# Kernel tuning notes

Measured on AMD Instinct MI355X. Metric: run time of the kernel, lower is better.

The kernel has to match this reference:

```python
import jax, jax.numpy as jnp
import numpy as np

DIM = 1024
N_HEADS = 16
HEAD_DIM = DIM // N_HEADS
SCALE = HEAD_DIM ** -0.5


def setup_inputs() -> dict:
    key = jax.random.key(0)
    ks = jax.random.split(key, 5)
    B, N = 2, 2048
    x = jax.random.normal(ks[0], (B, N, DIM), dtype=jnp.float32)
    # torch Linear: y = x @ W.T + b, W shape (out, in)
    qkv_w = jax.random.normal(ks[1], (3 * DIM, DIM), dtype=jnp.float32) * (DIM ** -0.5)
    qkv_b = jax.random.normal(ks[2], (3 * DIM,), dtype=jnp.float32) * 0.02
    proj_w = jax.random.normal(ks[3], (DIM, DIM), dtype=jnp.float32) * (DIM ** -0.5)
    proj_b = jax.random.normal(ks[4], (DIM,), dtype=jnp.float32) * 0.02
    return {"x": x, "qkv_w": qkv_w, "qkv_b": qkv_b, "proj_w": proj_w, "proj_b": proj_b}


def reference(x, qkv_w, qkv_b, proj_w, proj_b):
    B, N, D = x.shape
    qkv = x @ qkv_w.T + qkv_b                      # [B, N, 3D]
    qkv = qkv.reshape(B, N, 3, N_HEADS, HEAD_DIM)
    qkv = jnp.transpose(qkv, (2, 0, 3, 1, 4))      # [3, B, H, N, hd]
    q, k, v = qkv[0], qkv[1], qkv[2]
    dp = jnp.einsum('bhqd,bhkd->bhqk', q, k) * SCALE  # [B, H, N, N]
    attn = jax.nn.softmax(dp, axis=-1)
    wa = jnp.einsum('bhqk,bhkd->bhqd', attn, v)    # [B, H, N, hd]
    wa = jnp.transpose(wa, (0, 2, 1, 3)).reshape(B, N, D)
    return wa @ proj_w.T + proj_b
```

## Files before the change

kernel.cpp:

```cpp
#include <hip/hip_runtime.h>

#define BATCH 2
#define SEQ   2048
#define DIM   1024
#define NHEAD 16
#define HD    64
#define BH    (BATCH * NHEAD)
#define SCALE 0.125f
#define LOG2E 1.44269504f
#define NT    (SEQ / 64)

typedef __attribute__((ext_vector_type(8))) short short8;
typedef __attribute__((ext_vector_type(4))) float f32x4;

#define MFMA16(a, b, c) __builtin_amdgcn_mfma_f32_16x16x32_bf16(a, b, c, 0, 0, 0)

__device__ __forceinline__ ushort f2bf(float f) {
    union { float f; unsigned u; } v;
    v.f = f;
    unsigned r = (v.u + 0x7FFF + ((v.u >> 16) & 1)) >> 16;
    return (ushort)r;
}

__device__ __forceinline__ uint4 ld8f_bf16(const float* p) {
    float4 f0 = *(const float4*)p;
    float4 f1 = *(const float4*)(p + 4);
    union { ushort us[8]; uint4 v; } u;
    u.us[0] = f2bf(f0.x); u.us[1] = f2bf(f0.y);
    u.us[2] = f2bf(f0.z); u.us[3] = f2bf(f0.w);
    u.us[4] = f2bf(f1.x); u.us[5] = f2bf(f1.y);
    u.us[6] = f2bf(f1.z); u.us[7] = f2bf(f1.w);
    return u.v;
}

__device__ __forceinline__ void gl_lds16(const ushort* g, ushort* l) {
    __builtin_amdgcn_global_load_lds(
        (const __attribute__((address_space(1))) unsigned int*)g,
        (__attribute__((address_space(3))) unsigned int*)l,
        16, 0, 0);
}

#define N_X  (BATCH * SEQ * DIM)
#define N_QW (3 * DIM * DIM)
#define N_PW (DIM * DIM)

__global__ __launch_bounds__(256) void cvt_kernel(
    const float* __restrict__ x, const float* __restrict__ qw,
    const float* __restrict__ pw, ushort* __restrict__ xb,
    ushort* __restrict__ qwb, ushort* __restrict__ pwb)
{
    const int i = (blockIdx.x * 256 + threadIdx.x) * 8;
    if (i < N_X)  *(uint4*)(xb  + i) = ld8f_bf16(x  + i);
    if (i < N_QW) *(uint4*)(qwb + i) = ld8f_bf16(qw + i);
    if (i < N_PW) *(uint4*)(pwb + i) = ld8f_bf16(pw + i);
}

template <int MODE, int WM, typename TOUT>
__global__ __launch_bounds__(256, 2) void gemm_bt(
    const ushort* __restrict__ A, const ushort* __restrict__ W,
    const float* __restrict__ bias, TOUT* __restrict__ out,
    int M, int Nout, int K)
{
    constexpr int BM = 2 * WM * 16;
    __shared__ __align__(16) ushort As[2][BM * 32];
    __shared__ __align__(16) ushort Bs[2][128 * 32];

    const int tid  = threadIdx.x;
    const int wave = tid >> 6, lane = tid & 63;
    const int quad = lane >> 4, l16 = lane & 15;
    const int wm = wave >> 1, wn = wave & 1;
    const int m0 = blockIdx.y * BM, n0 = blockIdx.x * 128;

    const int c0 = tid, c1 = tid + 256;
    const ushort* gA0 = A + (size_t)(m0 + (c0 >> 2)) * K + (c0 & 3) * 8;
    const ushort* gA1 = A + (size_t)(m0 + (c1 >> 2)) * K + (c1 & 3) * 8;
    const ushort* gB0 = W + (size_t)(n0 + (c0 >> 2)) * K + (c0 & 3) * 8;
    const ushort* gB1 = W + (size_t)(n0 + (c1 >> 2)) * K + (c1 & 3) * 8;

#define STAGE_G(buf, k0)                                                  \
    {                                                                     \
        gl_lds16(gA0 + (k0), &As[buf][(wave * 64) * 8]);                  \
        if (WM == 4) gl_lds16(gA1 + (k0), &As[buf][(wave * 64 + 256) * 8]); \
        gl_lds16(gB0 + (k0), &Bs[buf][(wave * 64) * 8]);                  \
        gl_lds16(gB1 + (k0), &Bs[buf][(wave * 64 + 256) * 8]);            \
    }

    f32x4 acc[WM][4];
#pragma unroll
    for (int i = 0; i < WM; i++)
#pragma unroll
        for (int j = 0; j < 4; j++) acc[i][j] = (f32x4){0.f, 0.f, 0.f, 0.f};

    const int KT = K >> 5;
    STAGE_G(0, 0)

    for (int kt = 0; kt < KT; kt++) {
        const int cur = kt & 1;
        __syncthreads();
        if (kt + 1 < KT) STAGE_G(cur ^ 1, (kt + 1) * 32)

        short8 af[WM], bfr[4];
#pragma unroll
        for (int mt = 0; mt < WM; mt++)
            af[mt] = *(const short8*)&As[cur][(wm * (WM * 16) + mt * 16 + l16) * 32 + quad * 8];
#pragma unroll
        for (int nt = 0; nt < 4; nt++)
            bfr[nt] = *(const short8*)&Bs[cur][(wn * 64 + nt * 16 + l16) * 32 + quad * 8];
#pragma unroll
        for (int mt = 0; mt < WM; mt++)
#pragma unroll
            for (int nt = 0; nt < 4; nt++)
                acc[mt][nt] = MFMA16(af[mt], bfr[nt], acc[mt][nt]);
    }

#pragma unroll
    for (int nt = 0; nt < 4; nt++) {
        const int n = n0 + wn * 64 + nt * 16 + l16;
        const float bv = bias[n];
#pragma unroll
        for (int mt = 0; mt < WM; mt++) {
            const int mBase = m0 + wm * (WM * 16) + mt * 16 + quad * 4;
#pragma unroll
            for (int r = 0; r < 4; r++) {
                const int m = mBase + r;
                float v = acc[mt][nt][r] + bv;
                if (MODE == 0) {
                    const int which = n >> 10, rem = n & 1023;
                    const int h = rem >> 6, d = rem & 63;
                    const int b = m >> 11, nq = m & 2047;
                    const int bh = b * NHEAD + h;
                    if (which == 0) v *= (SCALE * LOG2E);
                    size_t idx;
                    if (which == 2)
                        idx = (size_t)2 * BH * SEQ * HD + ((size_t)bh * HD + d) * SEQ + nq;
                    else
                        idx = (size_t)which * BH * SEQ * HD + ((size_t)bh * SEQ + nq) * HD + d;
                    ((ushort*)out)[idx] = f2bf(v);
                } else {
                    ((float*)out)[(size_t)m * Nout + n] = v;
                }
            }
        }
    }
#undef STAGE_G
}

#define PSTR 72

__global__ __launch_bounds__(256, 2) void attn_kernel(
    const ushort* __restrict__ qkv, ushort* __restrict__ wa)
{
    __shared__ __align__(16) ushort Ks[2][64 * 64];
    __shared__ __align__(16) ushort Vs[2][64 * 64];
    __shared__ __align__(16) ushort Pb[4][32 * PSTR];

    const int tid  = threadIdx.x;
    const int wave = tid >> 6, lane = tid & 63;
    const int quad = lane >> 4, l16 = lane & 15;
    const int bh = blockIdx.y;
    const int b = bh >> 4, h = bh & 15;
    const size_t hOff = (size_t)bh * SEQ * HD;
    const ushort* Q  = qkv + hOff;
    const ushort* Kg = qkv + (size_t)BH * SEQ * HD + hOff;
    const ushort* Vt = qkv + (size_t)2 * BH * SEQ * HD + hOff;
    const int q0 = blockIdx.x * 128 + wave * 32;

    short8 aq[2][2];
#pragma unroll
    for (int mt = 0; mt < 2; mt++)
#pragma unroll
        for (int kh = 0; kh < 2; kh++)
            aq[mt][kh] = *(const short8*)&Q[(size_t)(q0 + mt * 16 + l16) * HD + kh * 32 + quad * 8];

    f32x4 o[2][4];
#pragma unroll
    for (int mt = 0; mt < 2; mt++)
#pragma unroll
        for (int dt = 0; dt < 4; dt++) o[mt][dt] = (f32x4){0.f, 0.f, 0.f, 0.f};
    float lsum[2][4];
#pragma unroll
    for (int mt = 0; mt < 2; mt++)
#pragma unroll
        for (int r = 0; r < 4; r++) lsum[mt][r] = 0.f;

    ushort* Pw = &Pb[wave][0];

    const int rr = lane >> 3;
    const int cc = ((lane & 7) ^ rr) * 8;
    const ushort* KgL = Kg + rr * HD + cc;
    const ushort* VtL = Vt + (size_t)rr * SEQ + cc;

#define STAGE(buf, kt)                                                       \
    {                                                                        \
        _Pragma("unroll")                                                    \
        for (int jj = 0; jj < 2; jj++) {                                     \
            const int j = wave * 2 + jj;                                     \
            gl_lds16(KgL + (size_t)((kt) * 64 + j * 8) * HD,                 \
                     &Ks[buf][j * 512]);                                     \
            gl_lds16(VtL + (size_t)(j * 8) * SEQ + (kt) * 64,                \
                     &Vs[buf][j * 512]);                                     \
        }                                                                    \
    }

    STAGE(0, 0)

    const int sw  = (l16 & 7);
    const int ko0 = (quad ^ sw) * 8;
    const int ko1 = ko0 ^ 32;

    for (int kt = 0; kt < NT; kt++) {
        const int cur = kt & 1;
        __syncthreads();
        if (kt + 1 < NT) STAGE(cur ^ 1, kt + 1)

        f32x4 s[2][4];
#pragma unroll
        for (int t = 0; t < 4; t++) {
            const ushort* kb = &Ks[cur][(t * 16 + l16) * 64];
            short8 bk0 = *(const short8*)&kb[ko0];
            short8 bk1 = *(const short8*)&kb[ko1];
#pragma unroll
            for (int mt = 0; mt < 2; mt++) {
                f32x4 z = (f32x4){0.f, 0.f, 0.f, 0.f};
                z = MFMA16(aq[mt][0], bk0, z);
                z = MFMA16(aq[mt][1], bk1, z);
                s[mt][t] = z;
            }
        }

#pragma unroll
        for (int mt = 0; mt < 2; mt++)
#pragma unroll
            for (int t = 0; t < 4; t++)
#pragma unroll
                for (int r = 0; r < 4; r++) {
                    const float pv = __builtin_amdgcn_exp2f(s[mt][t][r]);
                    s[mt][t][r] = pv;
                    lsum[mt][r] += pv;
                }

        short8 bv[4][2];
#pragma unroll
        for (int dt = 0; dt < 4; dt++) {
            const ushort* vb = &Vs[cur][(dt * 16 + l16) * 64];
            bv[dt][0] = *(const short8*)&vb[ko0];
            bv[dt][1] = *(const short8*)&vb[ko1];
        }

        __builtin_amdgcn_fence(__ATOMIC_ACQ_REL, "workgroup");
#pragma unroll
        for (int mt = 0; mt < 2; mt++)
#pragma unroll
            for (int t = 0; t < 4; t++)
#pragma unroll
                for (int r = 0; r < 4; r++)
                    Pw[(mt * 16 + quad * 4 + r) * PSTR + l16 + t * 16] = f2bf(s[mt][t][r]);
        __builtin_amdgcn_fence(__ATOMIC_ACQ_REL, "workgroup");

        short8 pa[2][2];
#pragma unroll
        for (int mt = 0; mt < 2; mt++) {
            pa[mt][0] = *(const short8*)&Pw[(mt * 16 + l16) * PSTR + quad * 8];
            pa[mt][1] = *(const short8*)&Pw[(mt * 16 + l16) * PSTR + 32 + quad * 8];
        }

#pragma unroll
        for (int mt = 0; mt < 2; mt++)
#pragma unroll
            for (int dt = 0; dt < 4; dt++) {
                o[mt][dt] = MFMA16(pa[mt][0], bv[dt][0], o[mt][dt]);
                o[mt][dt] = MFMA16(pa[mt][1], bv[dt][1], o[mt][dt]);
            }
    }

#pragma unroll
    for (int mt = 0; mt < 2; mt++)
#pragma unroll
        for (int r = 0; r < 4; r++) {
            float ssum = lsum[mt][r];
            ssum += __shfl_xor(ssum, 1);
            ssum += __shfl_xor(ssum, 2);
            ssum += __shfl_xor(ssum, 4);
            ssum += __shfl_xor(ssum, 8);
            lsum[mt][r] = ssum;
        }

#pragma unroll
    for (int mt = 0; mt < 2; mt++)
#pragma unroll
        for (int r = 0; r < 4; r++) {
            const float inv = 1.f / lsum[mt][r];
            const int qrow = q0 + mt * 16 + quad * 4 + r;
            ushort* dst = wa + ((size_t)(b * SEQ + qrow)) * DIM + h * HD;
#pragma unroll
            for (int dt = 0; dt < 4; dt++)
                dst[dt * 16 + l16] = f2bf(o[mt][dt][r] * inv);
        }
}

extern "C" void kernel_launch(void* const* d_in, const int* in_sizes, int n_in,
                              void* d_out, int out_size, void* d_ws, size_t ws_size,
                              hipStream_t stream)
{
    const float* x      = (const float*)d_in[0];
    const float* qkv_w  = (const float*)d_in[1];
    const float* qkv_b  = (const float*)d_in[2];
    const float* proj_w = (const float*)d_in[3];
    const float* proj_b = (const float*)d_in[4];
    float* out = (float*)d_out;

    ushort* xb  = (ushort*)d_ws;
    ushort* qwb = xb  + (size_t)N_X;
    ushort* pwb = qwb + (size_t)N_QW;
    ushort* qkv = pwb + (size_t)N_PW;
    ushort* wa  = qkv + (size_t)3 * BH * SEQ * HD;

    const int M = BATCH * SEQ;
    dim3 blk(256);

    cvt_kernel<<<dim3((N_X / 8 + 255) / 256), blk, 0, stream>>>(
        x, qkv_w, proj_w, xb, qwb, pwb);

    gemm_bt<0, 4, ushort><<<dim3((3 * DIM) / 128, M / 128), blk, 0, stream>>>(
        xb, qwb, qkv_b, qkv, M, 3 * DIM, DIM);

    attn_kernel<<<dim3(SEQ / 128, BH), blk, 0, stream>>>(qkv, wa);

    gemm_bt<1, 2, float><<<dim3(DIM / 128, M / 64), blk, 0, stream>>>(
        wa, pwb, proj_b, out, M, DIM, DIM);
}
```

Baseline: 206.1 us.

## Use 512-thread attention blocks with 16 query rows per wave and remapped grid

The attention kernel now runs 8 waves per block, each owning 16 query rows instead of 32. This halves per-wave accumulator and score registers and raises launch bounds to allow more resident waves. Each wave stages one K/V chunk instead of two, and a 1D grid remaps block indices so that consecutive blocks are spread across heads for locality and load balance. In exchange, each K/V tile loaded into LDS is reused by fewer MFMA operations per wave, and each wave issues relatively more synchronization.

After: 198.0 us. 1.04x faster.

```diff
diff --git a/kernel.cpp b/kernel.cpp
--- a/kernel.cpp
+++ b/kernel.cpp
@@ -147,41 +147,37 @@
 
 #define PSTR 72
 
-__global__ __launch_bounds__(256, 2) void attn_kernel(
+__global__ __launch_bounds__(512, 4) void attn_kernel(
     const ushort* __restrict__ qkv, ushort* __restrict__ wa)
 {
     __shared__ __align__(16) ushort Ks[2][64 * 64];
     __shared__ __align__(16) ushort Vs[2][64 * 64];
-    __shared__ __align__(16) ushort Pb[4][32 * PSTR];
+    __shared__ __align__(16) ushort Pb[8][16 * PSTR];
 
     const int tid  = threadIdx.x;
     const int wave = tid >> 6, lane = tid & 63;
     const int quad = lane >> 4, l16 = lane & 15;
-    const int bh = blockIdx.y;
+
+    const int l = blockIdx.x;
+    const int bh = (l & 7) + 8 * (l >> 7);
+    const int qi = (l >> 3) & 15;
     const int b = bh >> 4, h = bh & 15;
+
     const size_t hOff = (size_t)bh * SEQ * HD;
     const ushort* Q  = qkv + hOff;
     const ushort* Kg = qkv + (size_t)BH * SEQ * HD + hOff;
     const ushort* Vt = qkv + (size_t)2 * BH * SEQ * HD + hOff;
-    const int q0 = blockIdx.x * 128 + wave * 32;
-
-    short8 aq[2][2];
-#pragma unroll
-    for (int mt = 0; mt < 2; mt++)
-#pragma unroll
-        for (int kh = 0; kh < 2; kh++)
-            aq[mt][kh] = *(const short8*)&Q[(size_t)(q0 + mt * 16 + l16) * HD + kh * 32 + quad * 8];
-
-    f32x4 o[2][4];
-#pragma unroll
-    for (int mt = 0; mt < 2; mt++)
-#pragma unroll
-        for (int dt = 0; dt < 4; dt++) o[mt][dt] = (f32x4){0.f, 0.f, 0.f, 0.f};
-    float lsum[2][4];
-#pragma unroll
-    for (int mt = 0; mt < 2; mt++)
-#pragma unroll
-        for (int r = 0; r < 4; r++) lsum[mt][r] = 0.f;
+    const int q0 = qi * 128 + wave * 16;
+
+    short8 aq0 = *(const short8*)&Q[(size_t)(q0 + l16) * HD + quad * 8];
+    short8 aq1 = *(const short8*)&Q[(size_t)(q0 + l16) * HD + 32 + quad * 8];
+
+    f32x4 o[4];
+#pragma unroll
+    for (int dt = 0; dt < 4; dt++) o[dt] = (f32x4){0.f, 0.f, 0.f, 0.f};
+    float lsum[4];
+#pragma unroll
+    for (int r = 0; r < 4; r++) lsum[r] = 0.f;
 
     ushort* Pw = &Pb[wave][0];
 
@@ -192,14 +188,10 @@
 
 #define STAGE(buf, kt)                                                       \
     {                                                                        \
-        _Pragma("unroll")                                                    \
-        for (int jj = 0; jj < 2; jj++) {                                     \
-            const int j = wave * 2 + jj;                                     \
-            gl_lds16(KgL + (size_t)((kt) * 64 + j * 8) * HD,                 \
-                     &Ks[buf][j * 512]);                                     \
-            gl_lds16(VtL + (size_t)(j * 8) * SEQ + (kt) * 64,                \
-                     &Vs[buf][j * 512]);                                     \
-        }                                                                    \
+        gl_lds16(KgL + (size_t)((kt) * 64 + wave * 8) * HD,                  \
+                 &Ks[buf][wave * 512]);                                      \
+        gl_lds16(VtL + (size_t)(wave * 8) * SEQ + (kt) * 64,                 \
+                 &Vs[buf][wave * 512]);                                      \
     }
 
     STAGE(0, 0)
@@ -213,31 +205,26 @@
         __syncthreads();
         if (kt + 1 < NT) STAGE(cur ^ 1, kt + 1)
 
-        f32x4 s[2][4];
+        f32x4 s[4];
 #pragma unroll
         for (int t = 0; t < 4; t++) {
             const ushort* kb = &Ks[cur][(t * 16 + l16) * 64];
             short8 bk0 = *(const short8*)&kb[ko0];
             short8 bk1 = *(const short8*)&kb[ko1];
-#pragma unroll
-            for (int mt = 0; mt < 2; mt++) {
-                f32x4 z = (f32x4){0.f, 0.f, 0.f, 0.f};
-                z = MFMA16(aq[mt][0], bk0, z);
-                z = MFMA16(aq[mt][1], bk1, z);
-                s[mt][t] = z;
+            f32x4 z = (f32x4){0.f, 0.f, 0.f, 0.f};
+            z = MFMA16(aq0, bk0, z);
+            z = MFMA16(aq1, bk1, z);
+            s[t] = z;
+        }
+
+#pragma unroll
+        for (int t = 0; t < 4; t++)
+#pragma unroll
+            for (int r = 0; r < 4; r++) {
+                const float pv = __builtin_amdgcn_exp2f(s[t][r]);
+                s[t][r] = pv;
+                lsum[r] += pv;
             }
-        }
-
-#pragma unroll
-        for (int mt = 0; mt < 2; mt++)
-#pragma unroll
-            for (int t = 0; t < 4; t++)
-#pragma unroll
-                for (int r = 0; r < 4; r++) {
-                    const float pv = __builtin_amdgcn_exp2f(s[mt][t][r]);
-                    s[mt][t][r] = pv;
-                    lsum[mt][r] += pv;
-                }
 
         short8 bv[4][2];
 #pragma unroll
@@ -249,53 +236,41 @@
 
         __builtin_amdgcn_fence(__ATOMIC_ACQ_REL, "workgroup");
 #pragma unroll
-        for (int mt = 0; mt < 2; mt++)
-#pragma unroll
-            for (int t = 0; t < 4; t++)
-#pragma unroll
-                for (int r = 0; r < 4; r++)
-                    Pw[(mt * 16 + quad * 4 + r) * PSTR + l16 + t * 16] = f2bf(s[mt][t][r]);
+        for (int t = 0; t < 4; t++)
+#pragma unroll
+            for (int r = 0; r < 4; r++)
+                Pw[(quad * 4 + r) * PSTR + l16 + t * 16] = f2bf(s[t][r]);
         __builtin_amdgcn_fence(__ATOMIC_ACQ_REL, "workgroup");
 
-        short8 pa[2][2];
-#pragma unroll
-        for (int mt = 0; mt < 2; mt++) {
-            pa[mt][0] = *(const short8*)&Pw[(mt * 16 + l16) * PSTR + quad * 8];
-            pa[mt][1] = *(const short8*)&Pw[(mt * 16 + l16) * PSTR + 32 + quad * 8];
+        short8 pa0 = *(const short8*)&Pw[l16 * PSTR + quad * 8];
+        short8 pa1 = *(const short8*)&Pw[l16 * PSTR + 32 + quad * 8];
+
+#pragma unroll
+        for (int dt = 0; dt < 4; dt++) {
+            o[dt] = MFMA16(pa0, bv[dt][0], o[dt]);
+            o[dt] = MFMA16(pa1, bv[dt][1], o[dt]);
         }
-
-#pragma unroll
-        for (int mt = 0; mt < 2; mt++)
-#pragma unroll
-            for (int dt = 0; dt < 4; dt++) {
-                o[mt][dt] = MFMA16(pa[mt][0], bv[dt][0], o[mt][dt]);
-                o[mt][dt] = MFMA16(pa[mt][1], bv[dt][1], o[mt][dt]);
-            }
-    }
-
-#pragma unroll
-    for (int mt = 0; mt < 2; mt++)
-#pragma unroll
-        for (int r = 0; r < 4; r++) {
-            float ssum = lsum[mt][r];
-            ssum += __shfl_xor(ssum, 1);
-            ssum += __shfl_xor(ssum, 2);
-            ssum += __shfl_xor(ssum, 4);
-            ssum += __shfl_xor(ssum, 8);
-            lsum[mt][r] = ssum;
-        }
-
-#pragma unroll
-    for (int mt = 0; mt < 2; mt++)
-#pragma unroll
-        for (int r = 0; r < 4; r++) {
-            const float inv = 1.f / lsum[mt][r];
-            const int qrow = q0 + mt * 16 + quad * 4 + r;
-            ushort* dst = wa + ((size_t)(b * SEQ + qrow)) * DIM + h * HD;
-#pragma unroll
-            for (int dt = 0; dt < 4; dt++)
-                dst[dt * 16 + l16] = f2bf(o[mt][dt][r] * inv);
-        }
+    }
+
+#pragma unroll
+    for (int r = 0; r < 4; r++) {
+        float ssum = lsum[r];
+        ssum += __shfl_xor(ssum, 1);
+        ssum += __shfl_xor(ssum, 2);
+        ssum += __shfl_xor(ssum, 4);
+        ssum += __shfl_xor(ssum, 8);
+        lsum[r] = ssum;
+    }
+
+#pragma unroll
+    for (int r = 0; r < 4; r++) {
+        const float inv = 1.f / lsum[r];
+        const int qrow = q0 + quad * 4 + r;
+        ushort* dst = wa + ((size_t)(b * SEQ + qrow)) * DIM + h * HD;
+#pragma unroll
+        for (int dt = 0; dt < 4; dt++)
+            dst[dt * 16 + l16] = f2bf(o[dt][r] * inv);
+    }
 }
 
 extern "C" void kernel_launch(void* const* d_in, const int* in_sizes, int n_in,
@@ -324,7 +299,7 @@
     gemm_bt<0, 4, ushort><<<dim3((3 * DIM) / 128, M / 128), blk, 0, stream>>>(
         xb, qwb, qkv_b, qkv, M, 3 * DIM, DIM);
 
-    attn_kernel<<<dim3(SEQ / 128, BH), blk, 0, stream>>>(qkv, wa);
+    attn_kernel<<<dim3(512), dim3(512), 0, stream>>>(qkv, wa);
 
     gemm_bt<1, 2, float><<<dim3(DIM / 128, M / 64), blk, 0, stream>>>(
         wa, pwb, proj_b, out, M, DIM, DIM);
```

## Widen attention blocks to 8 waves, transpose S MFMA, pack P stores

Applied to the files above, without the earlier changes.

The attention kernel now uses 512-thread blocks covering 256 queries per head, so each staged K/V tile feeds twice as many waves. Blocks are remapped onto a 1D grid that groups heads. The QK^T MFMA swaps its operands so each lane holds four consecutive key scores of one query row. This lets P be written to LDS as packed bf16x2 uint2 stores and reduces the row-sum to one accumulator per tile plus two shuffles. The QKV and projection GEMMs raise their occupancy hint to 3 blocks per CU, which may force register spilling.

Result: slower. 215.7 us (+4.7%).

```diff
diff --git a/kernel.cpp b/kernel.cpp
--- a/kernel.cpp
+++ b/kernel.cpp
@@ -1,4 +1,5 @@
 #include <hip/hip_runtime.h>
+#include <hip/hip_bf16.h>
 
 #define BATCH 2
 #define SEQ   2048
@@ -22,6 +23,12 @@
     return (ushort)r;
 }
 
+__device__ __forceinline__ unsigned pk2bf(float a, float b) {
+    union { __hip_bfloat162 h; unsigned u; } v;
+    v.h = __float22bfloat162_rn(make_float2(a, b));
+    return v.u;
+}
+
 __device__ __forceinline__ uint4 ld8f_bf16(const float* p) {
     float4 f0 = *(const float4*)p;
     float4 f1 = *(const float4*)(p + 4);
@@ -56,7 +63,7 @@
 }
 
 template <int MODE, int WM, typename TOUT>
-__global__ __launch_bounds__(256, 2) void gemm_bt(
+__global__ __launch_bounds__(256, 3) void gemm_bt(
     const ushort* __restrict__ A, const ushort* __restrict__ W,
     const float* __restrict__ bias, TOUT* __restrict__ out,
     int M, int Nout, int K)
@@ -145,25 +152,29 @@
 #undef STAGE_G
 }
 
-#define PSTR 72
-
-__global__ __launch_bounds__(256, 2) void attn_kernel(
+#define PSTR 68
+
+__global__ __launch_bounds__(512, 2) void attn_kernel(
     const ushort* __restrict__ qkv, ushort* __restrict__ wa)
 {
     __shared__ __align__(16) ushort Ks[2][64 * 64];
     __shared__ __align__(16) ushort Vs[2][64 * 64];
-    __shared__ __align__(16) ushort Pb[4][32 * PSTR];
+    __shared__ __align__(16) ushort Pb[8][32 * PSTR];
 
     const int tid  = threadIdx.x;
     const int wave = tid >> 6, lane = tid & 63;
     const int quad = lane >> 4, l16 = lane & 15;
-    const int bh = blockIdx.y;
+
+    const int l = blockIdx.x;
+    const int bh = (l & 7) + 8 * (l >> 6);
+    const int qi = (l >> 3) & 7;
     const int b = bh >> 4, h = bh & 15;
+
     const size_t hOff = (size_t)bh * SEQ * HD;
     const ushort* Q  = qkv + hOff;
     const ushort* Kg = qkv + (size_t)BH * SEQ * HD + hOff;
     const ushort* Vt = qkv + (size_t)2 * BH * SEQ * HD + hOff;
-    const int q0 = blockIdx.x * 128 + wave * 32;
+    const int q0 = qi * 256 + wave * 32;
 
     short8 aq[2][2];
 #pragma unroll
@@ -177,11 +188,7 @@
     for (int mt = 0; mt < 2; mt++)
 #pragma unroll
         for (int dt = 0; dt < 4; dt++) o[mt][dt] = (f32x4){0.f, 0.f, 0.f, 0.f};
-    float lsum[2][4];
-#pragma unroll
-    for (int mt = 0; mt < 2; mt++)
-#pragma unroll
-        for (int r = 0; r < 4; r++) lsum[mt][r] = 0.f;
+    float lsum[2] = {0.f, 0.f};
 
     ushort* Pw = &Pb[wave][0];
 
@@ -192,14 +199,10 @@
 
 #define STAGE(buf, kt)                                                       \
     {                                                                        \
-        _Pragma("unroll")                                                    \
-        for (int jj = 0; jj < 2; jj++) {                                     \
-            const int j = wave * 2 + jj;                                     \
-            gl_lds16(KgL + (size_t)((kt) * 64 + j * 8) * HD,                 \
-                     &Ks[buf][j * 512]);                                     \
-            gl_lds16(VtL + (size_t)(j * 8) * SEQ + (kt) * 64,                \
-                     &Vs[buf][j * 512]);                                     \
-        }                                                                    \
+        gl_lds16(KgL + (size_t)((kt) * 64 + wave * 8) * HD,                  \
+                 &Ks[buf][wave * 512]);                                      \
+        gl_lds16(VtL + (size_t)(wave * 8) * SEQ + (kt) * 64,                 \
+                 &Vs[buf][wave * 512]);                                      \
     }
 
     STAGE(0, 0)
@@ -222,8 +225,8 @@
 #pragma unroll
             for (int mt = 0; mt < 2; mt++) {
                 f32x4 z = (f32x4){0.f, 0.f, 0.f, 0.f};
-                z = MFMA16(aq[mt][0], bk0, z);
-                z = MFMA16(aq[mt][1], bk1, z);
+                z = MFMA16(bk0, aq[mt][0], z);
+                z = MFMA16(bk1, aq[mt][1], z);
                 s[mt][t] = z;
             }
         }
@@ -236,7 +239,7 @@
                 for (int r = 0; r < 4; r++) {
                     const float pv = __builtin_amdgcn_exp2f(s[mt][t][r]);
                     s[mt][t][r] = pv;
-                    lsum[mt][r] += pv;
+                    lsum[mt] += pv;
                 }
 
         short8 bv[4][2];
@@ -251,10 +254,12 @@
 #pragma unroll
         for (int mt = 0; mt < 2; mt++)
 #pragma unroll
-            for (int t = 0; t < 4; t++)
-#pragma unroll
-                for (int r = 0; r < 4; r++)
-                    Pw[(mt * 16 + quad * 4 + r) * PSTR + l16 + t * 16] = f2bf(s[mt][t][r]);
+            for (int t = 0; t < 4; t++) {
+                uint2 pk;
+                pk.x = pk2bf(s[mt][t][0], s[mt][t][1]);
+                pk.y = pk2bf(s[mt][t][2], s[mt][t][3]);
+                *(uint2*)&Pw[(mt * 16 + l16) * PSTR + t * 16 + quad * 4] = pk;
+            }
         __builtin_amdgcn_fence(__ATOMIC_ACQ_REL, "workgroup");
 
         short8 pa[2][2];
@@ -274,22 +279,16 @@
     }
 
 #pragma unroll
+    for (int mt = 0; mt < 2; mt++) {
+        lsum[mt] += __shfl_xor(lsum[mt], 16);
+        lsum[mt] += __shfl_xor(lsum[mt], 32);
+    }
+
+#pragma unroll
     for (int mt = 0; mt < 2; mt++)
 #pragma unroll
         for (int r = 0; r < 4; r++) {
-            float ssum = lsum[mt][r];
-            ssum += __shfl_xor(ssum, 1);
-            ssum += __shfl_xor(ssum, 2);
-            ssum += __shfl_xor(ssum, 4);
-            ssum += __shfl_xor(ssum, 8);
-            lsum[mt][r] = ssum;
-        }
-
-#pragma unroll
-    for (int mt = 0; mt < 2; mt++)
-#pragma unroll
-        for (int r = 0; r < 4; r++) {
-            const float inv = 1.f / lsum[mt][r];
+            const float inv = 1.f / __shfl(lsum[mt], quad * 4 + r);
             const int qrow = q0 + mt * 16 + quad * 4 + r;
             ushort* dst = wa + ((size_t)(b * SEQ + qrow)) * DIM + h * HD;
 #pragma unroll
@@ -324,7 +323,7 @@
     gemm_bt<0, 4, ushort><<<dim3((3 * DIM) / 128, M / 128), blk, 0, stream>>>(
         xb, qwb, qkv_b, qkv, M, 3 * DIM, DIM);
 
-    attn_kernel<<<dim3(SEQ / 128, BH), blk, 0, stream>>>(qkv, wa);
+    attn_kernel<<<dim3(256), dim3(512), 0, stream>>>(qkv, wa);
 
     gemm_bt<1, 2, float><<<dim3(DIM / 128, M / 64), blk, 0, stream>>>(
         wa, pwb, proj_b, out, M, DIM, DIM);
```
